# Performance work log

Hardware: AMD Instinct MI355X
Metric: run time of the kernel (lower is better)

Reference implementation:

```python
import jax, jax.numpy as jnp
import numpy as np

B, S, H, TRK = 128, 256, 300, 64  # batch, seq tokens, hidden size, tracker size
N_STEPS = 2 * S - 1


def _valid_transitions(rng, batch, n_tok):
    """Random valid shift(0)/reduce(1) sequences of length 2*n_tok-1."""
    out = np.zeros((batch, 2 * n_tok - 1), dtype=np.int32)
    for b in range(batch):
        shifts_left, depth = n_tok, 0
        for i in range(2 * n_tok - 1):
            if depth < 2:
                a = 0
            elif shifts_left == 0:
                a = 1
            else:
                a = int(rng.integers(0, 2))
            out[b, i] = a
            if a == 0:
                shifts_left -= 1
                depth += 1
            else:
                depth -= 1
    return out


def setup_inputs() -> dict:
    key = jax.random.key(0)
    ks = jax.random.split(key, 12)
    sh = 1.0 / np.sqrt(H)
    st = 1.0 / np.sqrt(TRK)
    bufs = jax.random.normal(ks[0], (B, S, 2 * H), dtype=jnp.float32)
    transitions = jnp.asarray(_valid_transitions(np.random.default_rng(0), B, S))
    return {
        "bufs": bufs,
        "transitions": transitions,
        # tracker bundling projections (bias=False): Linear(size, 4*tracker)
        "W_buf": jax.random.uniform(ks[1], (H, 4 * TRK), jnp.float32, -sh, sh),
        "W_s1": jax.random.uniform(ks[2], (H, 4 * TRK), jnp.float32, -sh, sh),
        "W_s2": jax.random.uniform(ks[3], (H, 4 * TRK), jnp.float32, -sh, sh),
        # tracker LSTMCell(4*TRK, TRK, bias=False)
        "W_ih": jax.random.uniform(ks[4], (4 * TRK, 4 * TRK), jnp.float32, -st, st),
        "W_hh": jax.random.uniform(ks[5], (4 * TRK, TRK), jnp.float32, -st, st),
        # transition predictor Linear(TRK, 2)
        "W_trans": jax.random.uniform(ks[6], (TRK, 2), jnp.float32, -st, st),
        "b_trans": jax.random.uniform(ks[7], (2,), jnp.float32, -st, st),
        # Reduce (TreeLSTM composition, 5*H gates) with tracking input
        "W_left": jax.random.uniform(ks[8], (H, 5 * H), jnp.float32, -sh, sh),
        "W_right": jax.random.uniform(ks[9], (H, 5 * H), jnp.float32, -sh, sh),
        "W_track": jax.random.uniform(ks[10], (TRK, 5 * H), jnp.float32, -st, st),
        "b_reduce": jax.random.uniform(ks[11], (5 * H,), jnp.float32, -sh, sh),
    }


def reference(bufs, transitions, W_buf, W_s1, W_s2, W_ih, W_hh,
              W_trans, b_trans, W_left, W_right, W_track, b_reduce):
    Bn, Sn, D = bufs.shape
    Hn = D // 2  # element = concat(h, c)
    Tn = W_hh.shape[1]
    bidx = jnp.arange(Bn)

    stack0 = jnp.zeros((Bn, Sn + 1, D), dtype=bufs.dtype)
    carry0 = (stack0,
              jnp.zeros((Bn,), jnp.int32),          # stack ptr
              jnp.zeros((Bn,), jnp.int32),          # buffer ptr
              jnp.zeros((Bn, Tn), bufs.dtype),       # tracker h
              jnp.zeros((Bn, Tn), bufs.dtype))       # tracker c

    def gather(stack, ptr, off):
        el = stack[bidx, jnp.clip(ptr - off, 0)]
        return jnp.where((ptr >= off)[:, None], el, jnp.zeros_like(el))

    def step(carry, trans):
        stack, sptr, bptr, th, tc = carry
        buf_top = bufs[bidx, jnp.clip(bptr, 0, Sn - 1)]   # [B, 2H]
        s1 = gather(stack, sptr, 1)                        # stack[-1]
        s2 = gather(stack, sptr, 2)                        # stack[-2]
        # bundle h-parts -> tracker LSTM input (sum of three projections)
        lstm_in = buf_top[:, :Hn] @ W_buf + s1[:, :Hn] @ W_s1 + s2[:, :Hn] @ W_s2
        gates = lstm_in @ W_ih.T + th @ W_hh.T             # [B, 4T]
        gi, gf, gg, go = jnp.split(gates, 4, axis=1)       # torch LSTMCell order i,f,g,o
        tc = jax.nn.sigmoid(gf) * tc + jax.nn.sigmoid(gi) * jnp.tanh(gg)
        th = jax.nn.sigmoid(go) * jnp.tanh(tc)
        logits = th @ W_trans + b_trans                    # [B, 2]
        # TreeLSTM reduce: left = stack[-2], right = stack[-1]
        a = s2[:, :Hn] @ W_left + s1[:, :Hn] @ W_right + th @ W_track + b_reduce
        ri, fl, fr, ro, rg = jnp.split(a, 5, axis=1)
        rc = (jax.nn.sigmoid(fl) * s2[:, Hn:] + jax.nn.sigmoid(fr) * s1[:, Hn:]
              + jax.nn.sigmoid(ri) * jnp.tanh(rg))
        rh = jax.nn.sigmoid(ro) * jnp.tanh(rc)
        reduced = jnp.concatenate([rh, rc], axis=1)
        is_shift = (trans == 0)
        new_el = jnp.where(is_shift[:, None], buf_top, reduced)
        wpos = jnp.where(is_shift, sptr, jnp.clip(sptr - 2, 0))
        stack = stack.at[bidx, wpos].set(new_el)
        sptr = jnp.where(is_shift, sptr + 1, sptr - 1)
        bptr = bptr + is_shift.astype(jnp.int32)
        return (stack, sptr, bptr, th, tc), logits

    (stack, sptr, _, _, _), logits = jax.lax.scan(step, carry0, transitions.T)
    final_h = stack[bidx, jnp.clip(sptr - 1, 0)][:, :Hn]   # [B, H]
    # pack sentence encoding + per-step transition logits into one array
    return jnp.concatenate(
        [final_h, logits.transpose(1, 0, 2).reshape(Bn, -1)], axis=1)
```

## Files before the change

### kernel.cpp

```cpp
#include <hip/hip_runtime.h>


#define NSTEP 511
#define HB 128
#define SQ 256
#define HD 300
#define DW 600
#define TK 64

#define NB 16
#define NE 25
#define JPB 12
#define DOTS_E 60
#define KE 640
#define KLE 40
#define UPB 10
#define DOTS_T 40
#define KT 1008
#define KQT 21
#define KLT 48
#define ASTR 20
#define OUTW 1322

#define N_WEB 960000
#define N_WTB 282240
#define N_WTR 97500
#define N_TH  16384
#define N_STACK 19660800
#define N_BAR 1024
#define N_TPK 4096
#define N_WCT 230400

#define OFF_WEB 0
#define OFF_WTB 960000
#define OFF_WTR 1242240
#define OFF_TH  1339744
#define OFF_STACK 1356128
#define OFF_BAR 21016928
#define OFF_TPK 21017952
#define WS_FLOATS 21022048
#define OFF_WCT OFF_STACK

#define L_ACT 0
#define L_DUMP 20560
#define L_WTR 34000
#define L_THL 37900
#define L_BRED 38940
#define L_TRW 39004
#define L_INT 39520
#define LDS_FLOATS 39616

__device__ __forceinline__ float sigf(float x) { return 1.0f / (1.0f + __expf(-x)); }

__global__ void prep_a(const float* __restrict__ Wbuf, const float* __restrict__ Ws1,
                       const float* __restrict__ Ws2, const int* __restrict__ trans,
                       float* __restrict__ ws) {
  int idx = blockIdx.x * 256 + threadIdx.x;
  if (idx < N_WCT) {
    int k = idx % 900;
    int m = idx / 900;
    float v = (k < 300) ? Wbuf[k*256 + m]
            : (k < 600) ? Ws1[(k-300)*256 + m]
                        : Ws2[(k-600)*256 + m];
    ws[OFF_WCT + idx] = v;
    return;
  }
  idx -= N_WCT;
  if (idx < N_TH) { ws[OFF_TH + idx] = 0.0f; return; }
  idx -= N_TH;
  if (idx < N_BAR) { ws[OFF_BAR + idx] = 0.0f; return; }
  idx -= N_BAR;
  if (idx < 8*NSTEP) {
    int g = idx / NSTEP, t = idx % NSTEP;
    int w = 0;
    #pragma unroll
    for (int b = 0; b < 16; ++b)
      w |= (trans[(size_t)(g*16 + b)*NSTEP + t] & 1) << b;
    ((int*)(ws + OFF_TPK))[g*NSTEP + t] = w;
  }
}

__global__ void prep_b(const float* __restrict__ Wih, const float* __restrict__ Whh,
                       const float* __restrict__ Wl, const float* __restrict__ Wr,
                       const float* __restrict__ Wtrk, float* __restrict__ ws) {
  int idx = blockIdx.x * 256 + threadIdx.x;
  if (idx < N_WEB) {
    int k = idx % KE; int rest = idx / KE;
    int dot = rest % DOTS_E; int e = rest / DOTS_E;
    int g = dot / JPB, jj = dot % JPB;
    int col = g*HD + e*JPB + jj;
    float v = 0.0f;
    if (k < 300)      v = Wl[k*1500 + col];
    else if (k < 600) v = Wr[(k-300)*1500 + col];
    ws[OFF_WEB + idx] = v;
    return;
  }
  idx -= N_WEB;
  if (idx < N_WTB) {
    int k = idx % KT; int rest = idx / KT;
    int dot = rest % DOTS_T; int tb = rest / DOTS_T;
    int g = dot / UPB, uu = dot % UPB;
    int ucnt = (tb == 6) ? 10 : 9;
    float v = 0.0f;
    if (uu < ucnt) {
      int col = g*TK + tb*9 + uu;
      if (k < 900) {
        const float* wct = ws + OFF_WCT;
        const float* wi  = Wih + col*256;
        float s = 0.0f;
        #pragma unroll 4
        for (int m = 0; m < 256; ++m) s = fmaf(wct[m*900 + k], wi[m], s);
        v = s;
      } else if (k < 964) {
        v = Whh[col*TK + (k - 900)];
      }
    }
    ws[OFF_WTB + idx] = v;
    return;
  }
  idx -= N_WTB;
  if (idx < N_WTR) {
    int k = idx % 65; int rest = idx / 65;
    int dot = rest % DOTS_E; int e = rest / DOTS_E;
    int g = dot / JPB, jj = dot % JPB;
    ws[OFF_WTR + idx] = (k < 64) ? Wtrk[k*1500 + (g*HD + e*JPB + jj)] : 0.0f;
  }
}

__device__ __forceinline__ void xbar(int role, unsigned epoch,
                                     volatile unsigned* slots, volatile unsigned* flag,
                                     volatile int* broken) {
  __syncthreads();
  if (role == 0) {
    if (threadIdx.x < 64) {
      int lane = threadIdx.x;
      unsigned spins = 0;
      for (;;) {
        if (*broken) break;
        unsigned v = (lane >= 1 && lane < 32) ? slots[lane] : epoch;
        if (__all(v >= epoch)) break;
        __builtin_amdgcn_s_sleep(1);
        asm volatile("buffer_inv" ::: "memory");
        if (++spins > 2000000u) { if (lane == 0) *broken = 1; break; }
      }
      if (lane == 0) {
        *flag = epoch;
        asm volatile("s_waitcnt vmcnt(0)" ::: "memory");
      }
    }
  } else if (threadIdx.x == 0) {
    slots[role] = epoch;
    asm volatile("s_waitcnt vmcnt(0)" ::: "memory");
    unsigned spins = 0;
    while (!*broken && *flag < epoch) {
      __builtin_amdgcn_s_sleep(1);
      asm volatile("buffer_inv" ::: "memory");
      if (++spins > 2000000u) *broken = 1;
    }
  }
  __syncthreads();
  asm volatile("buffer_inv" ::: "memory");
}

template <int NC>
__device__ __forceinline__ void e_p1(const float* __restrict__ wb,
                                     const float* __restrict__ ab,
                                     float* __restrict__ dmp, int kq, int q) {
  float acc[4][4*NC];
  #pragma unroll
  for (int d = 0; d < 4; ++d)
    #pragma unroll
    for (int s = 0; s < 4*NC; ++s) acc[d][s] = 0.0f;

  #pragma unroll
  for (int i = 0; i < 10; ++i) {
    float wa[4][4];
    #pragma unroll
    for (int d = 0; d < 4; ++d) {
      float4 w = *(const float4*)(wb + (size_t)d*KE + 4*i);
      wa[d][0] = w.x; wa[d][1] = w.y; wa[d][2] = w.z; wa[d][3] = w.w;
    }
    #pragma unroll
    for (int kk = 0; kk < 4; ++kk) {
      const float* r = ab + (4*i + kk) * ASTR;
      #pragma unroll
      for (int c = 0; c < NC; ++c) {
        float4 a = *(const float4*)(r + 4*c);
        #pragma unroll
        for (int d = 0; d < 4; ++d) {
          acc[d][4*c+0] = fmaf(wa[d][kk], a.x, acc[d][4*c+0]);
          acc[d][4*c+1] = fmaf(wa[d][kk], a.y, acc[d][4*c+1]);
          acc[d][4*c+2] = fmaf(wa[d][kk], a.z, acc[d][4*c+2]);
          acc[d][4*c+3] = fmaf(wa[d][kk], a.w, acc[d][4*c+3]);
        }
      }
    }
  }
  #pragma unroll
  for (int d = 0; d < 4; ++d)
    #pragma unroll
    for (int s = 0; s < 4*NC; ++s)
      acc[d][s] += __shfl_xor(acc[d][s], 8, 64);
  if (kq < 8) {
    #pragma unroll
    for (int d = 0; d < 4; ++d)
      #pragma unroll
      for (int c = 0; c < NC; ++c)
        *(float4*)(dmp + ((size_t)(kq*DOTS_E + 4*q + d) * 16 + 4*c)) =
            make_float4(acc[d][4*c], acc[d][4*c+1], acc[d][4*c+2], acc[d][4*c+3]);
  }
}

__launch_bounds__(256, 1)
__global__ void spinn_kernel(const float* __restrict__ bufs,
                             const float* __restrict__ Wtrans, const float* __restrict__ btrans,
                             const float* __restrict__ bredv,
                             float* __restrict__ ws, float* __restrict__ out) {
  extern __shared__ float lds[];
  int* ibuf = (int*)(lds + L_INT);
  int* redl = ibuf + 16;
  int* shl  = ibuf + 32;
  int* sptr = ibuf + 48;
  int* bptr = ibuf + 64;
  volatile int* broken = ibuf + 82;
  int* role_s = ibuf + 90;
  int* trw = (int*)(lds + L_TRW);

  const int tid = threadIdx.x;

  unsigned xcc;
  asm volatile("s_getreg_b32 %0, hwreg(HW_REG_XCC_ID)" : "=s"(xcc));
  xcc &= 7u;
  if (tid == 0) {
    unsigned slot = __hip_atomic_fetch_add((unsigned*)(ws + OFF_BAR) + 512 + xcc, 1u,
                                           __ATOMIC_RELAXED, __HIP_MEMORY_SCOPE_AGENT);
    *role_s = (int)slot;
    *broken = 0;
  }
  __syncthreads();
  const int role = *role_s;
  const int group = (int)xcc;
  if (role >= 32) return;

  const int b0 = group * NB;
  const bool isE = (role < NE);
  const int e  = role;
  const int tb = role - NE;
  const int u0 = (tb >= 0) ? tb*9 : 0;
  const int ucnt = (tb == 6) ? 10 : 9;

  volatile unsigned* slots = (volatile unsigned*)((unsigned*)(ws + OFF_BAR) + (size_t)group*64);
  volatile unsigned* flag  = slots + 32;

  float* stack = ws + OFF_STACK;
  float* thbuf = ws + OFF_TH;

  float tc_reg = 0.0f;

  if (tid < 16) { sptr[tid] = 0; bptr[tid] = 0; }
  for (int i = tid; i < NSTEP; i += 256)
    trw[i] = ((const int*)(ws + OFF_TPK))[group*NSTEP + i];
  if (isE) {
    for (int i = tid; i < DOTS_E*65; i += 256)
      lds[L_WTR + i] = ws[OFF_WTR + (size_t)e*DOTS_E*65 + i];
    for (int i = tid; i < DOTS_E; i += 256)
      lds[L_BRED + i] = bredv[(i/JPB)*HD + e*JPB + (i%JPB)];
    for (int i = tid; i < 40*ASTR; i += 256) lds[L_ACT + 615*ASTR + i] = 0.0f;
  } else {
    for (int i = tid; i < 44*ASTR; i += 256) lds[L_ACT + 984*ASTR + i] = 0.0f;
  }
  __syncthreads();

  unsigned epoch = 0;

  for (int t = 0; t < NSTEP; ++t) {
    const int w = trw[t] & 0xFFFF;
    const int nred = __popc(w);
    if (tid < 16) {
      int rank = __popc(w & ((1u << tid) - 1u));
      if ((w >> tid) & 1) redl[rank] = tid; else shl[tid - rank] = tid;
    }
    __syncthreads();

    if (isE) {
      int r = tid >> 4, lane = tid & 15;
      if (r < nred) {
        int b = redl[r];
        int sp = sptr[b];
        const float* s2p = stack + ((size_t)((b0+b)*SQ + sp-2))*DW;
        const float* s1p = stack + ((size_t)((b0+b)*SQ + sp-1))*DW;
        #pragma unroll
        for (int i = 0; i < 10; ++i) {
          int ch = lane + 16*i;
          if (ch < 150) {
            int sec = ch / 75, kc = ch % 75;
            int dim = kc*4;
            const float* src = (sec == 0) ? s2p : s1p;
            float4 v = *(const float4*)(src + dim);
            int kbase = sec*300 + dim;
            int row0 = (kbase/40)*41 + (kbase%40);
            lds[L_ACT + (row0+0)*ASTR + r] = v.x;
            lds[L_ACT + (row0+1)*ASTR + r] = v.y;
            lds[L_ACT + (row0+2)*ASTR + r] = v.z;
            lds[L_ACT + (row0+3)*ASTR + r] = v.w;
          }
        }
      }
    } else {
      {
        int b = tid >> 4, lane = tid & 15;
        int bp = bptr[b]; if (bp > SQ-1) bp = SQ-1;
        int sp = sptr[b];
        const float* bsrc = bufs + ((size_t)((b0+b)*SQ + bp))*DW;
        const float* s1p = (sp >= 1) ? stack + ((size_t)((b0+b)*SQ + sp-1))*DW : nullptr;
        const float* s2p = (sp >= 2) ? stack + ((size_t)((b0+b)*SQ + sp-2))*DW : nullptr;
        #pragma unroll
        for (int i = 0; i < 15; ++i) {
          int ch = lane + 16*i;
          if (ch < 225) {
            int sec = ch / 75, kc = ch % 75;
            int dim = kc*4;
            const float* src = (sec == 0) ? bsrc : ((sec == 1) ? s1p : s2p);
            float4 v = make_float4(0.f, 0.f, 0.f, 0.f);
            if (src) v = *(const float4*)(src + dim);
            int kbase = sec*300 + dim;
            int row0 = (kbase/48)*49 + (kbase%48);
            lds[L_ACT + (row0+0)*ASTR + b] = v.x;
            lds[L_ACT + (row0+1)*ASTR + b] = v.y;
            lds[L_ACT + (row0+2)*ASTR + b] = v.z;
            lds[L_ACT + (row0+3)*ASTR + b] = v.w;
          }
        }
      }
      {
        int pm = (t - 1) & 1;
        int b = tid >> 4, uc = tid & 15;
        float4 v = *(const float4*)(thbuf + ((size_t)pm*HB + (b0+b))*TK + uc*4);
        float vv[4] = {v.x, v.y, v.z, v.w};
        #pragma unroll
        for (int l = 0; l < 4; ++l) {
          int k = 900 + uc*4 + l;
          int row = (k/48)*49 + (k%48);
          lds[L_ACT + row*ASTR + b] = vv[l];
        }
      }
    }
    __syncthreads();

    if (isE) {
      const int nchunk = (nred + 3) >> 2;
      if (nchunk > 0) {
        if (tid < 240) {
          int q = tid >> 4, kq = tid & 15;
          const float* wb = ws + OFF_WEB + (size_t)(e*DOTS_E + 4*q)*KE + kq*KLE;
          const float* ab = lds + L_ACT + (kq*41)*ASTR;
          if (nchunk <= 2) e_p1<2>(wb, ab, lds + L_DUMP, kq, q);
          else             e_p1<4>(wb, ab, lds + L_DUMP, kq, q);
        }
        __syncthreads();
        for (int task = tid; task < DOTS_E*16; task += 256) {
          int dot = task >> 4, s = task & 15;
          float sum = 0.0f;
          #pragma unroll
          for (int kq = 0; kq < 8; ++kq)
            sum += lds[L_DUMP + (size_t)(kq*DOTS_E + dot)*16 + s];
          lds[L_DUMP + (size_t)dot*16 + s] = sum;
        }
      }
    } else {
      if (tid < 210) {
        int q = tid / 21, kq = tid % 21;
        const float* wb = ws + OFF_WTB + (size_t)(tb*DOTS_T + 4*q)*KT + kq*KLT;
        const float* ab = lds + L_ACT + (kq*49)*ASTR;
        float acc[4][16];
        #pragma unroll
        for (int d = 0; d < 4; ++d)
          #pragma unroll
          for (int s = 0; s < 16; ++s) acc[d][s] = 0.0f;
        #pragma unroll 3
        for (int i = 0; i < 12; ++i) {
          float wa[4][4];
          #pragma unroll
          for (int d = 0; d < 4; ++d) {
            float4 w4 = *(const float4*)(wb + (size_t)d*KT + 4*i);
            wa[d][0] = w4.x; wa[d][1] = w4.y; wa[d][2] = w4.z; wa[d][3] = w4.w;
          }
          #pragma unroll
          for (int kk = 0; kk < 4; ++kk) {
            const float* r = ab + (4*i + kk) * ASTR;
            #pragma unroll
            for (int c = 0; c < 4; ++c) {
              float4 a = *(const float4*)(r + 4*c);
              #pragma unroll
              for (int d = 0; d < 4; ++d) {
                acc[d][4*c+0] = fmaf(wa[d][kk], a.x, acc[d][4*c+0]);
                acc[d][4*c+1] = fmaf(wa[d][kk], a.y, acc[d][4*c+1]);
                acc[d][4*c+2] = fmaf(wa[d][kk], a.z, acc[d][4*c+2]);
                acc[d][4*c+3] = fmaf(wa[d][kk], a.w, acc[d][4*c+3]);
              }
            }
          }
        }
        float* dmp = lds + L_DUMP;
        #pragma unroll
        for (int d = 0; d < 4; ++d)
          #pragma unroll
          for (int c = 0; c < 4; ++c)
            *(float4*)(dmp + ((size_t)(kq*DOTS_T + 4*q + d)*16 + 4*c)) =
                make_float4(acc[d][4*c], acc[d][4*c+1], acc[d][4*c+2], acc[d][4*c+3]);
      }
      __syncthreads();
      for (int task = tid; task < DOTS_T*16; task += 256) {
        int dot = task >> 4, s = task & 15;
        float sum = 0.0f;
        #pragma unroll
        for (int kq = 0; kq < KQT; ++kq)
          sum += lds[L_DUMP + (size_t)(kq*DOTS_T + dot)*16 + s];
        lds[L_DUMP + (size_t)dot*16 + s] = sum;
      }
      __syncthreads();
      if (tid < 160) {
        int uu = tid >> 4, b = tid & 15;
        if (uu < ucnt) {
          float gi = lds[L_DUMP + (size_t)(0*UPB + uu)*16 + b];
          float gf = lds[L_DUMP + (size_t)(1*UPB + uu)*16 + b];
          float gg = lds[L_DUMP + (size_t)(2*UPB + uu)*16 + b];
          float go = lds[L_DUMP + (size_t)(3*UPB + uu)*16 + b];
          tc_reg = sigf(gf)*tc_reg + sigf(gi)*tanhf(gg);
          float th = sigf(go)*tanhf(tc_reg);
          thbuf[((size_t)(t & 1)*HB + (b0 + b))*TK + (u0 + uu)] = th;
        }
      }
    }

    ++epoch;
    xbar(role, epoch, slots, flag, broken);

    if (isE) {
      int p = t & 1;
      {
        int r = tid >> 4, lane = tid & 15;
        if (r < nred) {
          const float* thp = thbuf + ((size_t)p*HB + (b0 + redl[r]))*TK;
          #pragma unroll
          for (int i = 0; i < 4; ++i) {
            int k = lane + 16*i;
            lds[L_THL + r*65 + k] = thp[k];
          }
        }
      }
      __syncthreads();
      if (tid < 192) {
        int rr = tid / JPB, jj = tid % JPB;
        int j = e*JPB + jj;
        if (rr < nred) {
          int b = redl[rr];
          int sp = sptr[b];
          float* s2base = stack + ((size_t)((b0+b)*SQ + (sp-2)))*DW;
          const float* s1base = stack + ((size_t)((b0+b)*SQ + (sp-1)))*DW;
          float s2c = s2base[HD + j];
          float s1c = s1base[HD + j];
          float a0 = lds[L_DUMP + (size_t)(0*JPB + jj)*16 + rr] + lds[L_BRED + 0*JPB + jj];
          float a1 = lds[L_DUMP + (size_t)(1*JPB + jj)*16 + rr] + lds[L_BRED + 1*JPB + jj];
          float a2 = lds[L_DUMP + (size_t)(2*JPB + jj)*16 + rr] + lds[L_BRED + 2*JPB + jj];
          float a3 = lds[L_DUMP + (size_t)(3*JPB + jj)*16 + rr] + lds[L_BRED + 3*JPB + jj];
          float a4 = lds[L_DUMP + (size_t)(4*JPB + jj)*16 + rr] + lds[L_BRED + 4*JPB + jj];
          #pragma unroll 8
          for (int k = 0; k < 64; ++k) {
            float tv = lds[L_THL + rr*65 + k];
            a0 = fmaf(tv, lds[L_WTR + (0*JPB + jj)*65 + k], a0);
            a1 = fmaf(tv, lds[L_WTR + (1*JPB + jj)*65 + k], a1);
            a2 = fmaf(tv, lds[L_WTR + (2*JPB + jj)*65 + k], a2);
            a3 = fmaf(tv, lds[L_WTR + (3*JPB + jj)*65 + k], a3);
            a4 = fmaf(tv, lds[L_WTR + (4*JPB + jj)*65 + k], a4);
          }
          float rc = sigf(a1)*s2c + sigf(a2)*s1c + sigf(a0)*tanhf(a4);
          float rh = sigf(a3)*tanhf(rc);
          s2base[j] = rh;
          s2base[HD + j] = rc;
        } else {
          int b = shl[rr - nred];
          int sp = sptr[b], bp = bptr[b];
          const float* src = bufs + ((size_t)((b0+b)*SQ + bp))*DW;
          float* dst = stack + ((size_t)((b0+b)*SQ + sp))*DW;
          dst[j] = src[j];
          dst[HD + j] = src[HD + j];
        }
      }
    } else if (role == NE) {
      if (tid < 32) {
        int b = tid >> 1, c = tid & 1;
        const float* th = thbuf + ((size_t)(t & 1)*HB + (b0 + b))*TK;
        float s = btrans[c];
        #pragma unroll 8
        for (int u = 0; u < TK; ++u) s = fmaf(th[u], Wtrans[u*2 + c], s);
        out[(size_t)(b0 + b)*OUTW + HD + 2*t + c] = s;
      }
    }

    __syncthreads();
    if (tid < 16) {
      if (!((w >> tid) & 1)) { sptr[tid] += 1; bptr[tid] += 1; }
      else                   { sptr[tid] -= 1; }
    }

    ++epoch;
    xbar(role, epoch, slots, flag, broken);
  }

  if (isE && tid < 192) {
    int b = tid / JPB, jj = tid % JPB;
    int j = e*JPB + jj;
    int sp = sptr[b] - 1; if (sp < 0) sp = 0;
    out[(size_t)(b0 + b)*OUTW + j] =
        stack[((size_t)((b0 + b)*SQ + sp))*DW + j];
  }
}

extern "C" void kernel_launch(void* const* d_in, const int* in_sizes, int n_in,
                              void* d_out, int out_size, void* d_ws, size_t ws_size,
                              hipStream_t stream) {
  const float* bufs   = (const float*)d_in[0];
  const int*   trans  = (const int*)  d_in[1];
  const float* Wbuf   = (const float*)d_in[2];
  const float* Ws1    = (const float*)d_in[3];
  const float* Ws2    = (const float*)d_in[4];
  const float* Wih    = (const float*)d_in[5];
  const float* Whh    = (const float*)d_in[6];
  const float* Wtrans = (const float*)d_in[7];
  const float* btrans = (const float*)d_in[8];
  const float* Wl     = (const float*)d_in[9];
  const float* Wr     = (const float*)d_in[10];
  const float* Wtrk   = (const float*)d_in[11];
  const float* bredv  = (const float*)d_in[12];
  float* ws  = (float*)d_ws;
  float* out = (float*)d_out;

  if (ws_size < (size_t)WS_FLOATS * sizeof(float)) return;

  {
    int total = N_WCT + N_TH + N_BAR + 8*NSTEP;
    prep_a<<<(total + 255) / 256, 256, 0, stream>>>(Wbuf, Ws1, Ws2, trans, ws);
  }
  {
    int total = N_WEB + N_WTB + N_WTR;
    prep_b<<<(total + 255) / 256, 256, 0, stream>>>(Wih, Whh, Wl, Wr, Wtrk, ws);
  }
  (void)hipFuncSetAttribute((const void*)spinn_kernel,
                            hipFuncAttributeMaxDynamicSharedMemorySize, 160000);
  spinn_kernel<<<256, 256, LDS_FLOATS * sizeof(float), stream>>>(
      bufs, Wtrans, btrans, bredv, ws, out);
}
```

Measured before the change: 12.17 ms.

## Keep per-thread weight slices resident in registers across all steps

Each thread loads its slice of the composition and tracker weights into a float4 register array once, before the step loop, so the 511 steps no longer reload those weights from global memory. The partial-sum dump buffers get padded strides (EDP/TDP) to reduce LDS bank conflicts. The cross-block barrier swaps volatile accesses plus buffer_inv for relaxed agent-scope atomics, and its spin timeout is doubled. The main risk is register pressure: 192 floats of weights per thread on top of the accumulators could cause spills.

```diff
diff --git a/kernel.cpp b/kernel.cpp
--- a/kernel.cpp
+++ b/kernel.cpp
@@ -17,7 +17,6 @@
 #define UPB 10
 #define DOTS_T 40
 #define KT 1008
-#define KQT 21
 #define KLT 48
 #define ASTR 20
 #define OUTW 1322
@@ -43,12 +42,14 @@
 
 #define L_ACT 0
 #define L_DUMP 20560
-#define L_WTR 34000
-#define L_THL 37900
-#define L_BRED 38940
-#define L_TRW 39004
-#define L_INT 39520
-#define LDS_FLOATS 39616
+#define EDP 964
+#define TDP 644
+#define L_WTR 34084
+#define L_THL 37984
+#define L_BRED 39024
+#define L_TRW 39088
+#define L_INT 39600
+#define LDS_FLOATS 39696
 
 __device__ __forceinline__ float sigf(float x) { return 1.0f / (1.0f + __expf(-x)); }
 
@@ -128,7 +129,7 @@
 }
 
 __device__ __forceinline__ void xbar(int role, unsigned epoch,
-                                     volatile unsigned* slots, volatile unsigned* flag,
+                                     unsigned* slots, unsigned* flag,
                                      volatile int* broken) {
   __syncthreads();
   if (role == 0) {
@@ -137,25 +138,23 @@
       unsigned spins = 0;
       for (;;) {
         if (*broken) break;
-        unsigned v = (lane >= 1 && lane < 32) ? slots[lane] : epoch;
+        unsigned v = (lane >= 1 && lane < 32)
+            ? __hip_atomic_load(slots + lane, __ATOMIC_RELAXED, __HIP_MEMORY_SCOPE_AGENT)
+            : epoch;
         if (__all(v >= epoch)) break;
         __builtin_amdgcn_s_sleep(1);
-        asm volatile("buffer_inv" ::: "memory");
-        if (++spins > 2000000u) { if (lane == 0) *broken = 1; break; }
-      }
-      if (lane == 0) {
-        *flag = epoch;
-        asm volatile("s_waitcnt vmcnt(0)" ::: "memory");
-      }
+        if (++spins > 4000000u) { if (lane == 0) *broken = 1; break; }
+      }
+      if (lane == 0)
+        __hip_atomic_store(flag, epoch, __ATOMIC_RELAXED, __HIP_MEMORY_SCOPE_AGENT);
     }
   } else if (threadIdx.x == 0) {
-    slots[role] = epoch;
-    asm volatile("s_waitcnt vmcnt(0)" ::: "memory");
+    __hip_atomic_store(slots + role, epoch, __ATOMIC_RELAXED, __HIP_MEMORY_SCOPE_AGENT);
     unsigned spins = 0;
-    while (!*broken && *flag < epoch) {
+    while (!*broken &&
+           __hip_atomic_load(flag, __ATOMIC_RELAXED, __HIP_MEMORY_SCOPE_AGENT) < epoch) {
       __builtin_amdgcn_s_sleep(1);
-      asm volatile("buffer_inv" ::: "memory");
-      if (++spins > 2000000u) *broken = 1;
+      if (++spins > 4000000u) *broken = 1;
     }
   }
   __syncthreads();
@@ -163,7 +162,7 @@
 }
 
 template <int NC>
-__device__ __forceinline__ void e_p1(const float* __restrict__ wb,
+__device__ __forceinline__ void e_p1(const float4 (&wf)[4][12],
                                      const float* __restrict__ ab,
                                      float* __restrict__ dmp, int kq, int q) {
   float acc[4][4*NC];
@@ -174,12 +173,6 @@
 
   #pragma unroll
   for (int i = 0; i < 10; ++i) {
-    float wa[4][4];
-    #pragma unroll
-    for (int d = 0; d < 4; ++d) {
-      float4 w = *(const float4*)(wb + (size_t)d*KE + 4*i);
-      wa[d][0] = w.x; wa[d][1] = w.y; wa[d][2] = w.z; wa[d][3] = w.w;
-    }
     #pragma unroll
     for (int kk = 0; kk < 4; ++kk) {
       const float* r = ab + (4*i + kk) * ASTR;
@@ -188,10 +181,12 @@
         float4 a = *(const float4*)(r + 4*c);
         #pragma unroll
         for (int d = 0; d < 4; ++d) {
-          acc[d][4*c+0] = fmaf(wa[d][kk], a.x, acc[d][4*c+0]);
-          acc[d][4*c+1] = fmaf(wa[d][kk], a.y, acc[d][4*c+1]);
-          acc[d][4*c+2] = fmaf(wa[d][kk], a.z, acc[d][4*c+2]);
-          acc[d][4*c+3] = fmaf(wa[d][kk], a.w, acc[d][4*c+3]);
+          float w = (kk == 0) ? wf[d][i].x : (kk == 1) ? wf[d][i].y
+                  : (kk == 2) ? wf[d][i].z : wf[d][i].w;
+          acc[d][4*c+0] = fmaf(w, a.x, acc[d][4*c+0]);
+          acc[d][4*c+1] = fmaf(w, a.y, acc[d][4*c+1]);
+          acc[d][4*c+2] = fmaf(w, a.z, acc[d][4*c+2]);
+          acc[d][4*c+3] = fmaf(w, a.w, acc[d][4*c+3]);
         }
       }
     }
@@ -206,7 +201,7 @@
     for (int d = 0; d < 4; ++d)
       #pragma unroll
       for (int c = 0; c < NC; ++c)
-        *(float4*)(dmp + ((size_t)(kq*DOTS_E + 4*q + d) * 16 + 4*c)) =
+        *(float4*)(dmp + kq*EDP + (4*q + d)*16 + 4*c) =
             make_float4(acc[d][4*c], acc[d][4*c+1], acc[d][4*c+2], acc[d][4*c+3]);
   }
 }
@@ -249,13 +244,36 @@
   const int u0 = (tb >= 0) ? tb*9 : 0;
   const int ucnt = (tb == 6) ? 10 : 9;
 
-  volatile unsigned* slots = (volatile unsigned*)((unsigned*)(ws + OFF_BAR) + (size_t)group*64);
-  volatile unsigned* flag  = slots + 32;
+  unsigned* slots = (unsigned*)(ws + OFF_BAR) + (size_t)group*64;
+  unsigned* flag  = slots + 32;
 
   float* stack = ws + OFF_STACK;
   float* thbuf = ws + OFF_TH;
 
   float tc_reg = 0.0f;
+
+  float4 wreg[4][12];
+  if (isE) {
+    if (tid < 240) {
+      const int q = tid >> 4, kq = tid & 15;
+      const float* wb = ws + OFF_WEB;
+      #pragma unroll
+      for (int d = 0; d < 4; ++d)
+        #pragma unroll
+        for (int i = 0; i < 10; ++i)
+          wreg[d][i] = *(const float4*)(wb + (size_t)(e*DOTS_E + 4*q + d)*KE + kq*KLE + 4*i);
+    }
+  } else {
+    if (tid < 210) {
+      const int q = tid / 21, kq = tid % 21;
+      const float* wb = ws + OFF_WTB;
+      #pragma unroll
+      for (int d = 0; d < 4; ++d)
+        #pragma unroll
+        for (int i = 0; i < 12; ++i)
+          wreg[d][i] = *(const float4*)(wb + (size_t)(tb*DOTS_T + 4*q + d)*KT + kq*KLT + 4*i);
+    }
+  }
 
   if (tid < 16) { sptr[tid] = 0; bptr[tid] = 0; }
   for (int i = tid; i < NSTEP; i += 256)
@@ -351,11 +369,10 @@
       const int nchunk = (nred + 3) >> 2;
       if (nchunk > 0) {
         if (tid < 240) {
-          int q = tid >> 4, kq = tid & 15;
-          const float* wb = ws + OFF_WEB + (size_t)(e*DOTS_E + 4*q)*KE + kq*KLE;
+          const int q = tid >> 4, kq = tid & 15;
           const float* ab = lds + L_ACT + (kq*41)*ASTR;
-          if (nchunk <= 2) e_p1<2>(wb, ab, lds + L_DUMP, kq, q);
-          else             e_p1<4>(wb, ab, lds + L_DUMP, kq, q);
+          if (nchunk <= 2) e_p1<2>(wreg, ab, lds + L_DUMP, kq, q);
+          else             e_p1<4>(wreg, ab, lds + L_DUMP, kq, q);
         }
         __syncthreads();
         for (int task = tid; task < DOTS_E*16; task += 256) {
@@ -363,28 +380,21 @@
           float sum = 0.0f;
           #pragma unroll
           for (int kq = 0; kq < 8; ++kq)
-            sum += lds[L_DUMP + (size_t)(kq*DOTS_E + dot)*16 + s];
-          lds[L_DUMP + (size_t)dot*16 + s] = sum;
+            sum += lds[L_DUMP + kq*EDP + dot*16 + s];
+          lds[L_DUMP + dot*16 + s] = sum;
         }
       }
     } else {
       if (tid < 210) {
-        int q = tid / 21, kq = tid % 21;
-        const float* wb = ws + OFF_WTB + (size_t)(tb*DOTS_T + 4*q)*KT + kq*KLT;
+        const int q = tid / 21, kq = tid % 21;
         const float* ab = lds + L_ACT + (kq*49)*ASTR;
         float acc[4][16];
         #pragma unroll
         for (int d = 0; d < 4; ++d)
           #pragma unroll
           for (int s = 0; s < 16; ++s) acc[d][s] = 0.0f;
-        #pragma unroll 3
+        #pragma unroll
         for (int i = 0; i < 12; ++i) {
-          float wa[4][4];
-          #pragma unroll
-          for (int d = 0; d < 4; ++d) {
-            float4 w4 = *(const float4*)(wb + (size_t)d*KT + 4*i);
-            wa[d][0] = w4.x; wa[d][1] = w4.y; wa[d][2] = w4.z; wa[d][3] = w4.w;
-          }
           #pragma unroll
           for (int kk = 0; kk < 4; ++kk) {
             const float* r = ab + (4*i + kk) * ASTR;
@@ -393,20 +403,22 @@
               float4 a = *(const float4*)(r + 4*c);
               #pragma unroll
               for (int d = 0; d < 4; ++d) {
-                acc[d][4*c+0] = fmaf(wa[d][kk], a.x, acc[d][4*c+0]);
-                acc[d][4*c+1] = fmaf(wa[d][kk], a.y, acc[d][4*c+1]);
-                acc[d][4*c+2] = fmaf(wa[d][kk], a.z, acc[d][4*c+2]);
-                acc[d][4*c+3] = fmaf(wa[d][kk], a.w, acc[d][4*c+3]);
+                float wv = (kk == 0) ? wreg[d][i].x : (kk == 1) ? wreg[d][i].y
+                         : (kk == 2) ? wreg[d][i].z : wreg[d][i].w;
+                acc[d][4*c+0] = fmaf(wv, a.x, acc[d][4*c+0]);
+                acc[d][4*c+1] = fmaf(wv, a.y, acc[d][4*c+1]);
+                acc[d][4*c+2] = fmaf(wv, a.z, acc[d][4*c+2]);
+                acc[d][4*c+3] = fmaf(wv, a.w, acc[d][4*c+3]);
               }
             }
           }
         }
-        float* dmp = lds + L_DUMP;
+        float* dmp = lds + L_DUMP + kq*TDP;
         #pragma unroll
         for (int d = 0; d < 4; ++d)
           #pragma unroll
           for (int c = 0; c < 4; ++c)
-            *(float4*)(dmp + ((size_t)(kq*DOTS_T + 4*q + d)*16 + 4*c)) =
+            *(float4*)(dmp + (4*q + d)*16 + 4*c) =
                 make_float4(acc[d][4*c], acc[d][4*c+1], acc[d][4*c+2], acc[d][4*c+3]);
       }
       __syncthreads();
@@ -414,18 +426,18 @@
         int dot = task >> 4, s = task & 15;
         float sum = 0.0f;
         #pragma unroll
-        for (int kq = 0; kq < KQT; ++kq)
-          sum += lds[L_DUMP + (size_t)(kq*DOTS_T + dot)*16 + s];
-        lds[L_DUMP + (size_t)dot*16 + s] = sum;
+        for (int kq = 0; kq < 21; ++kq)
+          sum += lds[L_DUMP + kq*TDP + dot*16 + s];
+        lds[L_DUMP + dot*16 + s] = sum;
       }
       __syncthreads();
       if (tid < 160) {
         int uu = tid >> 4, b = tid & 15;
         if (uu < ucnt) {
-          float gi = lds[L_DUMP + (size_t)(0*UPB + uu)*16 + b];
-          float gf = lds[L_DUMP + (size_t)(1*UPB + uu)*16 + b];
-          float gg = lds[L_DUMP + (size_t)(2*UPB + uu)*16 + b];
-          float go = lds[L_DUMP + (size_t)(3*UPB + uu)*16 + b];
+          float gi = lds[L_DUMP + (0*UPB + uu)*16 + b];
+          float gf = lds[L_DUMP + (1*UPB + uu)*16 + b];
+          float gg = lds[L_DUMP + (2*UPB + uu)*16 + b];
+          float go = lds[L_DUMP + (3*UPB + uu)*16 + b];
           tc_reg = sigf(gf)*tc_reg + sigf(gi)*tanhf(gg);
           float th = sigf(go)*tanhf(tc_reg);
           thbuf[((size_t)(t & 1)*HB + (b0 + b))*TK + (u0 + uu)] = th;
@@ -460,11 +472,11 @@
           const float* s1base = stack + ((size_t)((b0+b)*SQ + (sp-1)))*DW;
           float s2c = s2base[HD + j];
           float s1c = s1base[HD + j];
-          float a0 = lds[L_DUMP + (size_t)(0*JPB + jj)*16 + rr] + lds[L_BRED + 0*JPB + jj];
-          float a1 = lds[L_DUMP + (size_t)(1*JPB + jj)*16 + rr] + lds[L_BRED + 1*JPB + jj];
-          float a2 = lds[L_DUMP + (size_t)(2*JPB + jj)*16 + rr] + lds[L_BRED + 2*JPB + jj];
-          float a3 = lds[L_DUMP + (size_t)(3*JPB + jj)*16 + rr] + lds[L_BRED + 3*JPB + jj];
-          float a4 = lds[L_DUMP + (size_t)(4*JPB + jj)*16 + rr] + lds[L_BRED + 4*JPB + jj];
+          float a0 = lds[L_DUMP + (0*JPB + jj)*16 + rr] + lds[L_BRED + 0*JPB + jj];
+          float a1 = lds[L_DUMP + (1*JPB + jj)*16 + rr] + lds[L_BRED + 1*JPB + jj];
+          float a2 = lds[L_DUMP + (2*JPB + jj)*16 + rr] + lds[L_BRED + 2*JPB + jj];
+          float a3 = lds[L_DUMP + (3*JPB + jj)*16 + rr] + lds[L_BRED + 3*JPB + jj];
+          float a4 = lds[L_DUMP + (4*JPB + jj)*16 + rr] + lds[L_BRED + 4*JPB + jj];
           #pragma unroll 8
           for (int k = 0; k < 64; ++k) {
             float tv = lds[L_THL + rr*65 + k];
```

Measured after the change: 18.71 ms. +53.8%, slower.
